# Kernel tuning notes

Measured on AMD Instinct MI355X. Metric: run time of the kernel, lower is better.

Reference implementation:

```python
import jax, jax.numpy as jnp
import numpy as np

GRID = 64
BIG = 1.0e6  # threshold pushing masked-out pixels to huge distance


def _grid_dist(grid_h, grid_w):
    # pairwise euclidean distance between all grid points, (H, W, H, W)
    xs, ys = jnp.meshgrid(jnp.arange(grid_h), jnp.arange(grid_w), indexing='ij')
    coords = jnp.stack([xs.ravel(), ys.ravel()], axis=-1).astype(jnp.float32)  # (H*W, 2)
    d = jnp.sqrt(jnp.sum((coords[:, None, :] - coords[None, :, :]) ** 2, axis=-1))
    return d.reshape(grid_h, grid_w, grid_h, grid_w)


def setup_inputs() -> dict:
    key = jax.random.key(0)
    k1, k2 = jax.random.split(key)
    gt = jax.random.uniform(k1, (8, 64, 64), dtype=jnp.float32)
    pred = jax.random.uniform(k2, (8, 64, 64), dtype=jnp.float32)
    return {"gt": gt, "pred": pred}


def reference(gt, pred):
    # mode='l2_sq': sum over last axis (W for a (B,H,W) mask), then mean
    loss = jnp.mean(jnp.sum((gt - pred) ** 2, axis=-1))

    # affinity loss (dist_mat += 1.0 as in the original)
    dist = _grid_dist(GRID, GRID) + 1.0  # (64,64,64,64)

    gt_th = gt + (1.0 - gt) * BIG      # (B,H,W)
    pred_th = pred + (1.0 - pred) * BIG

    # dist_masked[b,h,w,i,j] = gt_th[b,h,w] * dist[h,w,i,j] * pred[b,i,j]
    dist_masked = gt_th[:, :, :, None, None] * dist[None] * pred[:, None, None, :, :]
    min_dist = jnp.mean(jnp.min(dist_masked, axis=(3, 4)))

    dist_masked_inv = pred_th[:, :, :, None, None] * dist[None] * gt[:, None, None, :, :]
    min_dist_inv = jnp.mean(jnp.min(dist_masked_inv, axis=(3, 4)))

    return (loss, min_dist, min_dist_inv)
```

## Files before the change

### kernel.cpp

```cpp
#include <hip/hip_runtime.h>

#define BIGV 1.0e6f

__global__ __launch_bounds__(256) void imageloss_main(
    const float* __restrict__ gt, const float* __restrict__ pred,
    float* __restrict__ ws)
{
    __shared__ float gt_s[4096];
    __shared__ float pr_s[4096];
    __shared__ float red1[256];
    __shared__ float red2[256];

    const int blk = blockIdx.x;
    const int b   = blk >> 6;
    const int h   = blk & 63;
    const int tid = threadIdx.x;

    const float* __restrict__ gt_b = gt   + b * 4096;
    const float* __restrict__ pr_b = pred + b * 4096;

    #pragma unroll
    for (int k = 0; k < 4; ++k) {
        int idx = tid + k * 256;
        ((float4*)gt_s)[idx] = ((const float4*)gt_b)[idx];
        ((float4*)pr_s)[idx] = ((const float4*)pr_b)[idx];
    }
    __syncthreads();

    const int w = tid & 63;
    const int c = tid >> 6;
    const float wf = (float)w;

    float m1 = 3.4e38f;
    float m2 = 3.4e38f;

    for (int i = c * 16; i < c * 16 + 16; ++i) {
        const float dxf = (float)(h - i);
        const float dx2 = dxf * dxf;
        const float4* __restrict__ pr4 = (const float4*)(pr_s + i * 64);
        const float4* __restrict__ gt4 = (const float4*)(gt_s + i * 64);
        #pragma unroll
        for (int j4 = 0; j4 < 16; ++j4) {
            float4 p4 = pr4[j4];
            float4 g4 = gt4[j4];
            #pragma unroll
            for (int t = 0; t < 4; ++t) {
                float jf = (float)(j4 * 4 + t);
                float dy = wf - jf;
                float d  = __builtin_amdgcn_sqrtf(fmaf(dy, dy, dx2));
                float p  = (&p4.x)[t];
                float g  = (&g4.x)[t];
                m1 = fminf(m1, fmaf(d, p, p));
                m2 = fminf(m2, fmaf(d, g, g));
            }
        }
    }

    red1[tid] = m1;
    red2[tid] = m2;
    __syncthreads();

    if (tid < 64) {
        m1 = fminf(fminf(red1[w], red1[64 + w]), fminf(red1[128 + w], red1[192 + w]));
        m2 = fminf(fminf(red2[w], red2[64 + w]), fminf(red2[128 + w], red2[192 + w]));

        const float g = gt_s[h * 64 + w];
        const float p = pr_s[h * 64 + w];
        const float gth = g + (1.0f - g) * BIGV;
        const float pth = p + (1.0f - p) * BIGV;

        float c1 = gth * m1;
        float c2 = pth * m2;
        float df = g - p;
        float sq = df * df;

        #pragma unroll
        for (int off = 32; off > 0; off >>= 1) {
            c1 += __shfl_down(c1, off, 64);
            c2 += __shfl_down(c2, off, 64);
            sq += __shfl_down(sq, off, 64);
        }
        if (w == 0) {
            atomicAdd(&ws[0], sq);
            atomicAdd(&ws[1], c1);
            atomicAdd(&ws[2], c2);
        }
    }
}

__global__ void imageloss_final(const float* __restrict__ ws, float* __restrict__ out)
{
    out[0] = ws[0] * (1.0f / 512.0f);
    out[1] = ws[1] * (1.0f / 32768.0f);
    out[2] = ws[2] * (1.0f / 32768.0f);
}

extern "C" void kernel_launch(void* const* d_in, const int* in_sizes, int n_in,
                              void* d_out, int out_size, void* d_ws, size_t ws_size,
                              hipStream_t stream)
{
    const float* gt   = (const float*)d_in[0];
    const float* pred = (const float*)d_in[1];
    float* out = (float*)d_out;
    float* ws  = (float*)d_ws;

    hipMemsetAsync(ws, 0, 3 * sizeof(float), stream);
    imageloss_main<<<512, 256, 0, stream>>>(gt, pred, ws);
    imageloss_final<<<1, 1, 0, stream>>>(ws, out);
}
```

Before: 46.75 us.

## Prune distance rows with per-row minimum lower bounds and outward row ordering

Computes per-row minimums of gt and pred while staging into shared memory, then visits candidate rows in order of increasing distance from h. Each wave skips rows whose lower bound (row distance plus one, times the row minimum) cannot beat the wave's current worst minimum. The aim is to cut most of the sqrt/fma/min work in the inner loop. In exchange it adds wave-wide max reductions and ballots on every iteration, and the loop trip count now depends on the data, which can cause divergence between waves.

```diff
diff --git a/kernel.cpp b/kernel.cpp
--- a/kernel.cpp
+++ b/kernel.cpp
@@ -1,6 +1,13 @@
 #include <hip/hip_runtime.h>
 
 #define BIGV 1.0e6f
+
+__device__ __forceinline__ float wave_max64(float v) {
+    #pragma unroll
+    for (int s = 32; s > 0; s >>= 1)
+        v = fmaxf(v, __shfl_xor(v, s, 64));
+    return v;
+}
 
 __global__ __launch_bounds__(256) void imageloss_main(
     const float* __restrict__ gt, const float* __restrict__ pred,
@@ -8,6 +15,8 @@
 {
     __shared__ float gt_s[4096];
     __shared__ float pr_s[4096];
+    __shared__ float rmg[64];
+    __shared__ float rmp[64];
     __shared__ float red1[256];
     __shared__ float red2[256];
 
@@ -22,8 +31,21 @@
     #pragma unroll
     for (int k = 0; k < 4; ++k) {
         int idx = tid + k * 256;
-        ((float4*)gt_s)[idx] = ((const float4*)gt_b)[idx];
-        ((float4*)pr_s)[idx] = ((const float4*)pr_b)[idx];
+        float4 vg = ((const float4*)gt_b)[idx];
+        float4 vp = ((const float4*)pr_b)[idx];
+        ((float4*)gt_s)[idx] = vg;
+        ((float4*)pr_s)[idx] = vp;
+        float mg = fminf(fminf(vg.x, vg.y), fminf(vg.z, vg.w));
+        float mp = fminf(fminf(vp.x, vp.y), fminf(vp.z, vp.w));
+        #pragma unroll
+        for (int s = 1; s < 16; s <<= 1) {
+            mg = fminf(mg, __shfl_xor(mg, s, 64));
+            mp = fminf(mp, __shfl_xor(mp, s, 64));
+        }
+        if ((tid & 15) == 0) {
+            rmg[idx >> 4] = mg;
+            rmp[idx >> 4] = mp;
+        }
     }
     __syncthreads();
 
@@ -31,12 +53,36 @@
     const int c = tid >> 6;
     const float wf = (float)w;
 
+    const int l     = w;
+    const int kcand = c + 4 * l;
+    const int offc  = (kcand & 1) ? ((kcand + 1) >> 1) : -(kcand >> 1);
+    const int rowc  = h + offc;
+    const bool valid = (l < 32) && (kcand <= 126) && ((unsigned)rowc < 64u);
+    float LB1 = 3.4e38f, LB2 = 3.4e38f;
+    if (valid) {
+        const int adx = offc < 0 ? -offc : offc;
+        const float dpl = (float)(adx + 1);
+        LB1 = dpl * rmp[rowc];
+        LB2 = dpl * rmg[rowc];
+    }
+    unsigned long long remaining = __ballot(valid);
+
     float m1 = 3.4e38f;
     float m2 = 3.4e38f;
 
-    for (int i = c * 16; i < c * 16 + 16; ++i) {
-        const float dxf = (float)(h - i);
-        const float dx2 = dxf * dxf;
+    while (remaining) {
+        const float T1 = wave_max64(m1);
+        const float T2 = wave_max64(m2);
+        unsigned long long need =
+            remaining & __ballot((LB1 < T1) || (LB2 < T2));
+        if (!need) break;
+        const int lsel = (int)__builtin_ctzll(need);
+        remaining &= ~(1ull << lsel);
+        const int ksel = c + 4 * lsel;
+        const int offs = (ksel & 1) ? ((ksel + 1) >> 1) : -(ksel >> 1);
+        const int i    = h + offs;
+        const float dx2 = (float)(offs * offs);
+
         const float4* __restrict__ pr4 = (const float4*)(pr_s + i * 64);
         const float4* __restrict__ gt4 = (const float4*)(gt_s + i * 64);
         #pragma unroll
@@ -61,16 +107,16 @@
     __syncthreads();
 
     if (tid < 64) {
-        m1 = fminf(fminf(red1[w], red1[64 + w]), fminf(red1[128 + w], red1[192 + w]));
-        m2 = fminf(fminf(red2[w], red2[64 + w]), fminf(red2[128 + w], red2[192 + w]));
+        float a1 = fminf(fminf(red1[w], red1[64 + w]), fminf(red1[128 + w], red1[192 + w]));
+        float a2 = fminf(fminf(red2[w], red2[64 + w]), fminf(red2[128 + w], red2[192 + w]));
 
         const float g = gt_s[h * 64 + w];
         const float p = pr_s[h * 64 + w];
         const float gth = g + (1.0f - g) * BIGV;
         const float pth = p + (1.0f - p) * BIGV;
 
-        float c1 = gth * m1;
-        float c2 = pth * m2;
+        float c1 = gth * a1;
+        float c2 = pth * a2;
         float df = g - p;
         float sq = df * df;
 
```

Measured after the change: 43.62 us. 1.07x faster.
